# Kernel optimization log

Measured on AMD Instinct MI355X. Metric: run time of the kernel, lower is better.

## Reference

```python
import jax, jax.numpy as jnp
import numpy as np

N, E, D_IN, D_OUT = 100000, 1600000, 128, 128
EPS = 1e-12  # torch F.normalize clamp


def setup_inputs() -> dict:
    key = jax.random.key(0)
    ks = jax.random.split(key, 8)
    return {
        "x": jax.random.normal(ks[0], (N, D_IN), dtype=jnp.float32),
        "edge_src": jax.random.randint(ks[1], (E,), 0, N, dtype=jnp.int32),
        "edge_dst": jax.random.randint(ks[2], (E,), 0, N, dtype=jnp.int32),
        "edge_weight": jax.random.uniform(ks[3], (E,), dtype=jnp.float32),
        "W_l": jax.random.normal(ks[4], (D_IN, D_OUT), dtype=jnp.float32) / np.sqrt(D_IN),
        "b_l": jax.random.normal(ks[5], (D_OUT,), dtype=jnp.float32) * 0.01,
        "W_r": jax.random.normal(ks[6], (D_IN, D_OUT), dtype=jnp.float32) / np.sqrt(D_IN),
        "b_r": jax.random.normal(ks[7], (D_OUT,), dtype=jnp.float32) * 0.01,
    }


def reference(x, edge_src, edge_dst, edge_weight, W_l, b_l, W_r, b_r):
    # spmm(adj, x): weighted gather of source node features, scatter-add to targets
    agg = jax.ops.segment_sum(x[edge_src] * edge_weight[:, None], edge_dst,
                              num_segments=x.shape[0])          # [N, D_IN]
    out = agg @ W_l + b_l + (x @ W_r + b_r)                      # lin_l + lin_r (num_tgt == N)
    # L1 normalize along features (F.normalize, p=1, dim=1)
    l1 = jnp.maximum(jnp.sum(jnp.abs(out), axis=1, keepdims=True), EPS)
    return out / l1
```

## Files before the change

kernel.cpp:

```cpp
#include <hip/hip_runtime.h>
#include <hip/hip_fp16.h>


static constexpr int D = 128;
static constexpr int CBITS = 6;
static constexpr int CSZ = 1 << CBITS;
static constexpr int NB = 2048;
static constexpr int NPART = 256;

typedef _Float16 half8 __attribute__((ext_vector_type(8)));
typedef float f32x4 __attribute__((ext_vector_type(4)));

__global__ __launch_bounds__(256) void prep(
    const int* __restrict__ edst, int* __restrict__ bhist, int E, int chunk,
    const float4* __restrict__ x4, __half2* __restrict__ xh2, int n4,
    const float* __restrict__ Wl, const float* __restrict__ Wr,
    __half* __restrict__ wt, int do_cvt)
{
    __shared__ int hist[NB];
    const int b = blockIdx.x;
    const int tid = threadIdx.x;
    if (b < NPART) {
        for (int t = tid; t < NB; t += 256) hist[t] = 0;
        __syncthreads();
        const int beg = b * chunk;
        const int end = min(E, beg + chunk);
        int e = beg + tid;
        for (; e + 3 * 256 < end; e += 4 * 256) {
            const int d0 = edst[e];
            const int d1 = edst[e + 256];
            const int d2 = edst[e + 512];
            const int d3 = edst[e + 768];
            atomicAdd(&hist[d0 >> CBITS], 1);
            atomicAdd(&hist[d1 >> CBITS], 1);
            atomicAdd(&hist[d2 >> CBITS], 1);
            atomicAdd(&hist[d3 >> CBITS], 1);
        }
        for (; e < end; e += 256)
            atomicAdd(&hist[edst[e] >> CBITS], 1);
        __syncthreads();
        for (int t = tid; t < NB; t += 256)
            bhist[(size_t)b * NB + t] = hist[t];
    } else if (do_cvt) {
        const int cb = b - NPART;
        if (cb < 1024) {
            int i = cb * 256 + tid;
            const int stride = 1024 * 256;
            for (; i < n4; i += stride) {
                float4 v = x4[i];
                xh2[2 * i + 0] = __floats2half2_rn(v.x, v.y);
                xh2[2 * i + 1] = __floats2half2_rn(v.z, v.w);
            }
        } else {
            const int idx = (cb - 1024) * 256 + tid;
            if (idx < 128 * 256) {
                const int c = idx >> 8;
                const int k = idx & 255;
                const float v = (k < 128) ? Wl[(size_t)k * D + c]
                                          : Wr[(size_t)(k - 128) * D + c];
                wt[(size_t)c * 256 + k] = __float2half(v);
            }
        }
    }
}

__global__ __launch_bounds__(64) void bucket_scan(
    int* __restrict__ bhist, int* __restrict__ ctot)
{
    const int t = blockIdx.x * 64 + threadIdx.x;
    int run = 0;
    for (int b = 0; b < NPART; b += 8) {
        int v[8];
#pragma unroll
        for (int i = 0; i < 8; ++i)
            v[i] = bhist[(size_t)(b + i) * NB + t];
#pragma unroll
        for (int i = 0; i < 8; ++i) {
            const int c = v[i];
            bhist[(size_t)(b + i) * NB + t] = run;
            run += c;
        }
    }
    ctot[t] = run;
}

__global__ __launch_bounds__(1024) void coarse_scan(
    const int* __restrict__ ctot, int* __restrict__ cbase,
    int* __restrict__ offs, int N, int E)
{
    __shared__ int s[1024];
    const int t = threadIdx.x;
    const int v0 = ctot[2 * t];
    const int v1 = ctot[2 * t + 1];
    const int loc = v0 + v1;
    s[t] = loc;
    __syncthreads();
    for (int off = 1; off < 1024; off <<= 1) {
        const int u = (t >= off) ? s[t - off] : 0;
        __syncthreads();
        s[t] += u;
        __syncthreads();
    }
    const int excl = s[t] - loc;
    cbase[2 * t]     = excl;
    cbase[2 * t + 1] = excl + v0;
    if (t == 1023) { cbase[NB] = s[t]; offs[N] = E; }
}

__global__ __launch_bounds__(256) void coarse_partition(
    const int* __restrict__ esrc, const int* __restrict__ edst,
    const float* __restrict__ ew, const int* __restrict__ bhist,
    const int* __restrict__ cbase,
    int2* __restrict__ cpairs, int E, int chunk)
{
    __shared__ int cur[NB];
    for (int t = threadIdx.x; t < NB; t += 256)
        cur[t] = bhist[(size_t)blockIdx.x * NB + t] + cbase[t];
    __syncthreads();
    const int beg = blockIdx.x * chunk;
    const int end = min(E, beg + chunk);
    int e = beg + threadIdx.x;
    for (; e + 3 * 256 < end; e += 4 * 256) {
        int d_[4], s_[4]; float w_[4];
#pragma unroll
        for (int i = 0; i < 4; ++i) {
            d_[i] = edst[e + i * 256];
            s_[i] = esrc[e + i * 256];
            w_[i] = ew[e + i * 256];
        }
#pragma unroll
        for (int i = 0; i < 4; ++i) {
            const int pos = atomicAdd(&cur[d_[i] >> CBITS], 1);
            cpairs[pos] = make_int2(((d_[i] & (CSZ - 1)) << 20) | s_[i],
                                    __float_as_int(w_[i]));
        }
    }
    for (; e < end; e += 256) {
        const int d = edst[e];
        const int pos = atomicAdd(&cur[d >> CBITS], 1);
        cpairs[pos] = make_int2(((d & (CSZ - 1)) << 20) | esrc[e],
                                __float_as_int(ew[e]));
    }
}

__global__ __launch_bounds__(256) void fine_sort(
    const int2* __restrict__ cpairs, const int* __restrict__ cbase,
    int* __restrict__ offs, int2* __restrict__ pairs, int N)
{
    __shared__ int hist[CSZ], scn[CSZ], cur[CSZ];
    const int b = blockIdx.x;
    const int t = threadIdx.x;
    const int lane = t & 63;
    const int s0 = cbase[b], s1 = cbase[b + 1];
    if (t < CSZ) hist[t] = 0;
    __syncthreads();
    for (int i = s0 + t; i < s1; i += 256)
        atomicAdd(&hist[(cpairs[i].x >> 20) & (CSZ - 1)], 1);
    __syncthreads();
    if (t < CSZ) {
        const int v = hist[t];
        int xs = v;
#pragma unroll
        for (int off = 1; off < 64; off <<= 1) {
            const int y = __shfl_up(xs, off, 64);
            if (lane >= off) xs += y;
        }
        const int base = s0 + xs - v;
        scn[t] = base;
        cur[t] = base;
        const int node = (b << CBITS) + t;
        if (node < N) offs[node] = base;
    }
    __syncthreads();
    for (int i = s0 + t; i < s1; i += 256) {
        const int2 p = cpairs[i];
        const int pos = atomicAdd(&cur[(p.x >> 20) & (CSZ - 1)], 1);
        pairs[pos] = make_int2(p.x & 0xFFFFF, p.y);
    }
}

template <bool FP16X>
__global__ __launch_bounds__(256) void sage_gather(
    const void* __restrict__ xrows,
    const int2* __restrict__ pairs,
    const int* __restrict__ offs,
    void* __restrict__ agg,
    int N)
{
    int node = (blockIdx.x * blockDim.x + threadIdx.x) >> 6;
    const int lane = threadIdx.x & 63;
    if (node >= N) return;
    node = __builtin_amdgcn_readfirstlane(node);
    const int beg = offs[node];
    const int end = offs[node + 1];
    const int sub = lane >> 5;
    const int cl  = lane & 31;

    const __half* __restrict__ xh = (const __half*)xrows;
    const float*  __restrict__ xf = (const float*)xrows;

    float a0 = 0.f, a1 = 0.f, a2 = 0.f, a3 = 0.f;
    int k = beg;
    for (; k + 8 <= end; k += 8) {
        int s_[4]; float w_[4];
#pragma unroll
        for (int i = 0; i < 4; ++i) {
            const int2 ea = pairs[k + 2 * i + 0];
            const int2 eb = pairs[k + 2 * i + 1];
            s_[i] = sub ? eb.x : ea.x;
            w_[i] = __int_as_float(sub ? eb.y : ea.y);
        }
        if (FP16X) {
            float2 raw[4];
#pragma unroll
            for (int i = 0; i < 4; ++i)
                raw[i] = *reinterpret_cast<const float2*>(&xh[(size_t)s_[i] * D + cl * 4]);
#pragma unroll
            for (int i = 0; i < 4; ++i) {
                union { float2 f2; __half2 h[2]; } u;
                u.f2 = raw[i];
                const float2 f01 = __half22float2(u.h[0]);
                const float2 f23 = __half22float2(u.h[1]);
                a0 = fmaf(f01.x, w_[i], a0);
                a1 = fmaf(f01.y, w_[i], a1);
                a2 = fmaf(f23.x, w_[i], a2);
                a3 = fmaf(f23.y, w_[i], a3);
            }
        } else {
            float4 raw[4];
#pragma unroll
            for (int i = 0; i < 4; ++i)
                raw[i] = *reinterpret_cast<const float4*>(&xf[(size_t)s_[i] * D + cl * 4]);
#pragma unroll
            for (int i = 0; i < 4; ++i) {
                a0 = fmaf(raw[i].x, w_[i], a0);
                a1 = fmaf(raw[i].y, w_[i], a1);
                a2 = fmaf(raw[i].z, w_[i], a2);
                a3 = fmaf(raw[i].w, w_[i], a3);
            }
        }
    }
    for (int t = 0; k + t < end; ++t) {
        if (sub == (t & 1)) {
            const int2 p = pairs[k + t];
            const float w = __int_as_float(p.y);
            if (FP16X) {
                union { float2 f2; __half2 h[2]; } u;
                u.f2 = *reinterpret_cast<const float2*>(&xh[(size_t)p.x * D + cl * 4]);
                const float2 f01 = __half22float2(u.h[0]);
                const float2 f23 = __half22float2(u.h[1]);
                a0 = fmaf(f01.x, w, a0); a1 = fmaf(f01.y, w, a1);
                a2 = fmaf(f23.x, w, a2); a3 = fmaf(f23.y, w, a3);
            } else {
                const float4 v = *reinterpret_cast<const float4*>(&xf[(size_t)p.x * D + cl * 4]);
                a0 = fmaf(v.x, w, a0); a1 = fmaf(v.y, w, a1);
                a2 = fmaf(v.z, w, a2); a3 = fmaf(v.w, w, a3);
            }
        }
    }
    a0 += __shfl_xor(a0, 32, 64);
    a1 += __shfl_xor(a1, 32, 64);
    a2 += __shfl_xor(a2, 32, 64);
    a3 += __shfl_xor(a3, 32, 64);

    if (sub == 0) {
        if (FP16X) {
            union { __half2 h[2]; int2 i2; } u;
            u.h[0] = __floats2half2_rn(a0, a1);
            u.h[1] = __floats2half2_rn(a2, a3);
            *reinterpret_cast<int2*>(&((__half*)agg)[(size_t)node * D + cl * 4]) = u.i2;
        } else {
            *reinterpret_cast<float4*>(&((float*)agg)[(size_t)node * D + cl * 4]) =
                make_float4(a0, a1, a2, a3);
        }
    }
}

__global__ __launch_bounds__(256) void sage_scatter(
    const float* __restrict__ x,
    const int* __restrict__ esrc,
    const int* __restrict__ edst,
    const float* __restrict__ ew,
    float* agg, int E)
{
    const int lane = threadIdx.x & 63;
    const int warp = (blockIdx.x * blockDim.x + threadIdx.x) >> 6;
    const int nwarps = (gridDim.x * blockDim.x) >> 6;
    const float2* __restrict__ x2 = reinterpret_cast<const float2*>(x);
    for (int e = warp; e < E; e += nwarps) {
        const int s = esrc[e];
        const int d = edst[e];
        const float w = ew[e];
        const float2 xv = x2[s * 64 + lane];
        atomicAdd(&agg[d * D + lane * 2 + 0], xv.x * w);
        atomicAdd(&agg[d * D + lane * 2 + 1], xv.y * w);
    }
}

__global__ __launch_bounds__(256) void sage_linear_norm_mfma(
    const __half* __restrict__ aggh,
    const __half* __restrict__ xh,
    const __half* __restrict__ wt,
    const float* __restrict__ bl,
    const float* __restrict__ br,
    float* __restrict__ out,
    int N)
{
    __shared__ __half a_s[64][136];
    __shared__ __half w_s[128][136];
    const int tid = threadIdx.x;
    const int bn = blockIdx.x * 64;
    const int wv = tid >> 6;
    const int l  = tid & 63;
    const int lr = l & 15;
    const int lq = l >> 4;

    f32x4 acc[8];
#pragma unroll
    for (int t = 0; t < 8; ++t) acc[t] = f32x4{0.f, 0.f, 0.f, 0.f};

    const int ar  = tid >> 2;
    const int as  = (tid & 3) * 32;
    const int wr  = tid >> 1;
    const int wsg = (tid & 1) * 64;

#pragma unroll
    for (int c = 0; c < 2; ++c) {
        const __half* __restrict__ A = c ? xh : aggh;
        __syncthreads();
        {
            const int gn = bn + ar;
            half8 v0 = {}, v1 = {}, v2 = {}, v3 = {};
            if (gn < N) {
                const half8* src = reinterpret_cast<const half8*>(&A[(size_t)gn * D + as]);
                v0 = src[0]; v1 = src[1]; v2 = src[2]; v3 = src[3];
            }
            half8* dst = reinterpret_cast<half8*>(&a_s[ar][as]);
            dst[0] = v0; dst[1] = v1; dst[2] = v2; dst[3] = v3;
        }
        {
            const half8* src = reinterpret_cast<const half8*>(&wt[(size_t)wr * 256 + c * 128 + wsg]);
            half8* dst = reinterpret_cast<half8*>(&w_s[wr][wsg]);
#pragma unroll
            for (int j = 0; j < 8; ++j) dst[j] = src[j];
        }
        __syncthreads();

#pragma unroll
        for (int ks = 0; ks < 4; ++ks) {
            const int k0 = ks * 32 + lq * 8;
            const half8 af = *reinterpret_cast<const half8*>(&a_s[wv * 16 + lr][k0]);
#pragma unroll
            for (int t = 0; t < 8; ++t) {
                const half8 bf = *reinterpret_cast<const half8*>(&w_s[t * 16 + lr][k0]);
                acc[t] = __builtin_amdgcn_mfma_f32_16x16x32_f16(af, bf, acc[t], 0, 0, 0);
            }
        }
    }

    float bias[8];
#pragma unroll
    for (int t = 0; t < 8; ++t) {
        const int cidx = t * 16 + lr;
        bias[t] = bl[cidx] + br[cidx];
    }
    float v[8][4];
    float s0 = 0.f, s1 = 0.f, s2 = 0.f, s3 = 0.f;
#pragma unroll
    for (int t = 0; t < 8; ++t) {
        v[t][0] = acc[t][0] + bias[t];
        v[t][1] = acc[t][1] + bias[t];
        v[t][2] = acc[t][2] + bias[t];
        v[t][3] = acc[t][3] + bias[t];
        s0 += fabsf(v[t][0]); s1 += fabsf(v[t][1]);
        s2 += fabsf(v[t][2]); s3 += fabsf(v[t][3]);
    }
#pragma unroll
    for (int m = 1; m < 16; m <<= 1) {
        s0 += __shfl_xor(s0, m, 64);
        s1 += __shfl_xor(s1, m, 64);
        s2 += __shfl_xor(s2, m, 64);
        s3 += __shfl_xor(s3, m, 64);
    }
    const float r0 = 1.0f / fmaxf(s0, 1e-12f);
    const float r1 = 1.0f / fmaxf(s1, 1e-12f);
    const float r2 = 1.0f / fmaxf(s2, 1e-12f);
    const float r3 = 1.0f / fmaxf(s3, 1e-12f);

    const int nd0 = bn + wv * 16 + lq * 4;
#pragma unroll
    for (int r = 0; r < 4; ++r) {
        const int nd = nd0 + r;
        if (nd < N) {
            const float ri = (r == 0) ? r0 : (r == 1) ? r1 : (r == 2) ? r2 : r3;
#pragma unroll
            for (int t = 0; t < 8; ++t)
                out[(size_t)nd * D + t * 16 + lr] = v[t][r] * ri;
        }
    }
}

__global__ __launch_bounds__(256) void sage_linear_norm(
    const float* agg, const float* __restrict__ x,
    const float* __restrict__ Wl, const float* __restrict__ bl,
    const float* __restrict__ Wr, const float* __restrict__ br,
    float* out, int N)
{
    __shared__ float a_s[64][68];
    __shared__ float w_s[64][132];
    const int tid = threadIdx.x;
    const int jg = tid & 31;
    const int ng = tid >> 5;
    const int bn = blockIdx.x * 64;

    float acc[8][4];
#pragma unroll
    for (int i = 0; i < 8; ++i) {
        acc[i][0] = 0.f; acc[i][1] = 0.f; acc[i][2] = 0.f; acc[i][3] = 0.f;
    }
    const int sn  = tid >> 2;
    const int skb = (tid & 3) << 4;
    const int wr  = tid >> 5;
    const int wc  = (tid & 31) << 2;

    for (int c = 0; c < 4; ++c) {
        const float* A = (c < 2) ? agg : x;
        const float* __restrict__ W = (c < 2) ? Wl : Wr;
        const int kb = (c & 1) << 6;
        __syncthreads();
        const int gn = bn + sn;
#pragma unroll
        for (int it = 0; it < 4; ++it) {
            float4 vv = make_float4(0.f, 0.f, 0.f, 0.f);
            if (gn < N)
                vv = *reinterpret_cast<const float4*>(&A[(size_t)gn * D + kb + skb + it * 4]);
            *reinterpret_cast<float4*>(&a_s[sn][skb + it * 4]) = vv;
        }
#pragma unroll
        for (int it = 0; it < 8; ++it) {
            const int row = it * 8 + wr;
            const float4 vv = *reinterpret_cast<const float4*>(&W[(size_t)(kb + row) * D + wc]);
            *reinterpret_cast<float4*>(&w_s[row][wc]) = vv;
        }
        __syncthreads();
#pragma unroll 4
        for (int kk = 0; kk < 64; kk += 4) {
            const float4 w0 = *reinterpret_cast<const float4*>(&w_s[kk + 0][jg << 2]);
            const float4 w1 = *reinterpret_cast<const float4*>(&w_s[kk + 1][jg << 2]);
            const float4 w2 = *reinterpret_cast<const float4*>(&w_s[kk + 2][jg << 2]);
            const float4 w3 = *reinterpret_cast<const float4*>(&w_s[kk + 3][jg << 2]);
#pragma unroll
            for (int i = 0; i < 8; ++i) {
                const float4 av = *reinterpret_cast<const float4*>(&a_s[(ng << 3) + i][kk]);
                acc[i][0] = fmaf(av.w, w3.x, fmaf(av.z, w2.x, fmaf(av.y, w1.x, fmaf(av.x, w0.x, acc[i][0]))));
                acc[i][1] = fmaf(av.w, w3.y, fmaf(av.z, w2.y, fmaf(av.y, w1.y, fmaf(av.x, w0.y, acc[i][1]))));
                acc[i][2] = fmaf(av.w, w3.z, fmaf(av.z, w2.z, fmaf(av.y, w1.z, fmaf(av.x, w0.z, acc[i][2]))));
                acc[i][3] = fmaf(av.w, w3.w, fmaf(av.z, w2.w, fmaf(av.y, w1.w, fmaf(av.x, w0.w, acc[i][3]))));
            }
        }
    }
    const float4 bl4 = *reinterpret_cast<const float4*>(&bl[jg << 2]);
    const float4 br4 = *reinterpret_cast<const float4*>(&br[jg << 2]);
    const float bx = bl4.x + br4.x, by = bl4.y + br4.y,
                bz = bl4.z + br4.z, bw = bl4.w + br4.w;
#pragma unroll
    for (int i = 0; i < 8; ++i) {
        const float v0 = acc[i][0] + bx;
        const float v1 = acc[i][1] + by;
        const float v2 = acc[i][2] + bz;
        const float v3 = acc[i][3] + bw;
        float s = fabsf(v0) + fabsf(v1) + fabsf(v2) + fabsf(v3);
#pragma unroll
        for (int m = 1; m < 32; m <<= 1) s += __shfl_xor(s, m, 64);
        s = fmaxf(s, 1e-12f);
        const float r = 1.0f / s;
        const int n = bn + (ng << 3) + i;
        if (n < N) {
            const float4 o = make_float4(v0 * r, v1 * r, v2 * r, v3 * r);
            *reinterpret_cast<float4*>(&out[(size_t)n * D + (jg << 2)]) = o;
        }
    }
}

extern "C" void kernel_launch(void* const* d_in, const int* in_sizes, int n_in,
                              void* d_out, int out_size, void* d_ws, size_t ws_size,
                              hipStream_t stream) {
    const float* x    = (const float*)d_in[0];
    const int*   esrc = (const int*)  d_in[1];
    const int*   edst = (const int*)  d_in[2];
    const float* ew   = (const float*)d_in[3];
    const float* Wl   = (const float*)d_in[4];
    const float* bl   = (const float*)d_in[5];
    const float* Wr   = (const float*)d_in[6];
    const float* br   = (const float*)d_in[7];
    float* out = (float*)d_out;

    const int N = in_sizes[0] / D;
    const int E = in_sizes[1];

    auto align256 = [](size_t v) { return (v + 255) & ~size_t(255); };
    size_t off_bhist  = 0;
    size_t off_ctot   = align256(off_bhist  + (size_t)NPART * NB * 4);
    size_t off_cbase  = align256(off_ctot   + (size_t)NB * 4);
    size_t off_offs   = align256(off_cbase  + (size_t)(NB + 1) * 4);
    size_t off_cpairs = align256(off_offs   + (size_t)(N + 1) * 4);
    size_t off_pairs  = align256(off_cpairs + (size_t)E * 8);
    size_t off_xh     = align256(off_pairs  + (size_t)E * 8);
    size_t off_aggh   = align256(off_xh     + (size_t)N * D * 2);
    size_t off_wt     = align256(off_aggh   + (size_t)N * D * 2);
    size_t need_b     = off_xh;
    size_t need_a     = off_wt + (size_t)256 * D * 2;

    const int nbu = (N + CSZ - 1) >> CBITS;
    const bool fits_meta = (N <= (1 << 20)) && (nbu <= NB);

    if (ws_size >= need_b && fits_meta) {
        char* ws = (char*)d_ws;
        int*  bhist  = (int*) (ws + off_bhist);
        int*  ctot   = (int*) (ws + off_ctot);
        int*  cbase  = (int*) (ws + off_cbase);
        int*  offs   = (int*) (ws + off_offs);
        int2* cpairs = (int2*)(ws + off_cpairs);
        int2* pairs  = (int2*)(ws + off_pairs);
        __half2* xh  = (__half2*)(ws + off_xh);
        __half*  agh = (__half*)(ws + off_aggh);
        __half*  wt  = (__half*)(ws + off_wt);

        const bool mfma = (ws_size >= need_a);
        const int chunk = (E + NPART - 1) / NPART;

        const int prep_grid = NPART + (mfma ? (1024 + 128) : 0);
        prep<<<prep_grid, 256, 0, stream>>>(edst, bhist, E, chunk,
                                            (const float4*)x, xh, N * (D / 4),
                                            Wl, Wr, wt, mfma ? 1 : 0);
        bucket_scan<<<NB / 64, 64, 0, stream>>>(bhist, ctot);
        coarse_scan<<<1, 1024, 0, stream>>>(ctot, cbase, offs, N, E);
        coarse_partition<<<NPART, 256, 0, stream>>>(esrc, edst, ew, bhist, cbase,
                                                    cpairs, E, chunk);
        fine_sort<<<nbu, 256, 0, stream>>>(cpairs, cbase, offs, pairs, N);

        const int gb = (N * 64 + 255) / 256;
        const int nb = (N + 63) / 64;
        if (mfma) {
            sage_gather<true ><<<gb, 256, 0, stream>>>(xh, pairs, offs, agh, N);
            sage_linear_norm_mfma<<<nb, 256, 0, stream>>>(agh, (const __half*)xh, wt,
                                                          bl, br, out, N);
        } else {
            sage_gather<false><<<gb, 256, 0, stream>>>(x, pairs, offs, out, N);
            sage_linear_norm<<<nb, 256, 0, stream>>>(out, x, Wl, bl, Wr, br, out, N);
        }
    } else {
        hipMemsetAsync(out, 0, (size_t)N * D * sizeof(float), stream);
        sage_scatter<<<2048, 256, 0, stream>>>(x, esrc, edst, ew, out, E);
        const int nb = (N + 63) / 64;
        sage_linear_norm<<<nb, 256, 0, stream>>>(out, x, Wl, bl, Wr, br, out, N);
    }
}
```

Measured before the change: 149.3 us.

## Use full-wave row gather per edge and wave-shuffle scan in coarse_scan

The gather kernel now has all 64 lanes cooperate on one source row per edge, each lane loading a half2 or float2, instead of splitting the wave into two half-waves that each handle alternate edges with 4-wide loads. This drops the cross-half shuffle reduction and the per-lane edge selection, at the cost of narrower per-lane loads and one row in flight per edge step. The coarse scan replaces a shared-memory Hillis-Steele scan that needed many barriers with wave-level shuffle scans plus one small scan over wave sums. The scan kernel is tiny, so most of the effect depends on how the gather's memory access pattern changes.

Result: faster. 146.0 us, median of 2 (-2.2%).

```diff
diff --git a/kernel.cpp b/kernel.cpp
--- a/kernel.cpp
+++ b/kernel.cpp
@@ -88,23 +88,36 @@
     const int* __restrict__ ctot, int* __restrict__ cbase,
     int* __restrict__ offs, int N, int E)
 {
-    __shared__ int s[1024];
+    __shared__ int wsum[16];
     const int t = threadIdx.x;
+    const int lane = t & 63;
+    const int wv = t >> 6;
     const int v0 = ctot[2 * t];
     const int v1 = ctot[2 * t + 1];
     const int loc = v0 + v1;
-    s[t] = loc;
+    int xs = loc;
+#pragma unroll
+    for (int off = 1; off < 64; off <<= 1) {
+        const int y = __shfl_up(xs, off, 64);
+        if (lane >= off) xs += y;
+    }
+    if (lane == 63) wsum[wv] = xs;
     __syncthreads();
-    for (int off = 1; off < 1024; off <<= 1) {
-        const int u = (t >= off) ? s[t - off] : 0;
-        __syncthreads();
-        s[t] += u;
-        __syncthreads();
-    }
-    const int excl = s[t] - loc;
+    if (t < 16) {
+        const int w = wsum[t];
+        int ws = w;
+#pragma unroll
+        for (int off = 1; off < 16; off <<= 1) {
+            const int y = __shfl_up(ws, off, 64);
+            if (lane >= off) ws += y;
+        }
+        wsum[t] = ws - w;
+    }
+    __syncthreads();
+    const int excl = wsum[wv] + xs - loc;
     cbase[2 * t]     = excl;
     cbase[2 * t + 1] = excl + v0;
-    if (t == 1023) { cbase[NB] = s[t]; offs[N] = E; }
+    if (t == 1023) { cbase[NB] = excl + loc; offs[N] = E; }
 }
 
 __global__ __launch_bounds__(256) void coarse_partition(
@@ -193,86 +206,50 @@
     node = __builtin_amdgcn_readfirstlane(node);
     const int beg = offs[node];
     const int end = offs[node + 1];
-    const int sub = lane >> 5;
-    const int cl  = lane & 31;
-
-    const __half* __restrict__ xh = (const __half*)xrows;
-    const float*  __restrict__ xf = (const float*)xrows;
-
-    float a0 = 0.f, a1 = 0.f, a2 = 0.f, a3 = 0.f;
+
+    const __half2* __restrict__ xh = (const __half2*)xrows;
+    const float2*  __restrict__ xf = (const float2*)xrows;
+
+    float ax0 = 0.f, ay0 = 0.f, ax1 = 0.f, ay1 = 0.f;
     int k = beg;
-    for (; k + 8 <= end; k += 8) {
-        int s_[4]; float w_[4];
-#pragma unroll
-        for (int i = 0; i < 4; ++i) {
-            const int2 ea = pairs[k + 2 * i + 0];
-            const int2 eb = pairs[k + 2 * i + 1];
-            s_[i] = sub ? eb.x : ea.x;
-            w_[i] = __int_as_float(sub ? eb.y : ea.y);
-        }
+    for (; k + 4 <= end; k += 4) {
+        const int2 p0 = pairs[k + 0];
+        const int2 p1 = pairs[k + 1];
+        const int2 p2 = pairs[k + 2];
+        const int2 p3 = pairs[k + 3];
+        float2 v0, v1, v2, v3;
         if (FP16X) {
-            float2 raw[4];
-#pragma unroll
-            for (int i = 0; i < 4; ++i)
-                raw[i] = *reinterpret_cast<const float2*>(&xh[(size_t)s_[i] * D + cl * 4]);
-#pragma unroll
-            for (int i = 0; i < 4; ++i) {
-                union { float2 f2; __half2 h[2]; } u;
-                u.f2 = raw[i];
-                const float2 f01 = __half22float2(u.h[0]);
-                const float2 f23 = __half22float2(u.h[1]);
-                a0 = fmaf(f01.x, w_[i], a0);
-                a1 = fmaf(f01.y, w_[i], a1);
-                a2 = fmaf(f23.x, w_[i], a2);
-                a3 = fmaf(f23.y, w_[i], a3);
-            }
+            v0 = __half22float2(xh[(size_t)p0.x * 64 + lane]);
+            v1 = __half22float2(xh[(size_t)p1.x * 64 + lane]);
+            v2 = __half22float2(xh[(size_t)p2.x * 64 + lane]);
+            v3 = __half22float2(xh[(size_t)p3.x * 64 + lane]);
         } else {
-            float4 raw[4];
-#pragma unroll
-            for (int i = 0; i < 4; ++i)
-                raw[i] = *reinterpret_cast<const float4*>(&xf[(size_t)s_[i] * D + cl * 4]);
-#pragma unroll
-            for (int i = 0; i < 4; ++i) {
-                a0 = fmaf(raw[i].x, w_[i], a0);
-                a1 = fmaf(raw[i].y, w_[i], a1);
-                a2 = fmaf(raw[i].z, w_[i], a2);
-                a3 = fmaf(raw[i].w, w_[i], a3);
-            }
-        }
-    }
-    for (int t = 0; k + t < end; ++t) {
-        if (sub == (t & 1)) {
-            const int2 p = pairs[k + t];
-            const float w = __int_as_float(p.y);
-            if (FP16X) {
-                union { float2 f2; __half2 h[2]; } u;
-                u.f2 = *reinterpret_cast<const float2*>(&xh[(size_t)p.x * D + cl * 4]);
-                const float2 f01 = __half22float2(u.h[0]);
-                const float2 f23 = __half22float2(u.h[1]);
-                a0 = fmaf(f01.x, w, a0); a1 = fmaf(f01.y, w, a1);
-                a2 = fmaf(f23.x, w, a2); a3 = fmaf(f23.y, w, a3);
-            } else {
-                const float4 v = *reinterpret_cast<const float4*>(&xf[(size_t)p.x * D + cl * 4]);
-                a0 = fmaf(v.x, w, a0); a1 = fmaf(v.y, w, a1);
-                a2 = fmaf(v.z, w, a2); a3 = fmaf(v.w, w, a3);
-            }
-        }
-    }
-    a0 += __shfl_xor(a0, 32, 64);
-    a1 += __shfl_xor(a1, 32, 64);
-    a2 += __shfl_xor(a2, 32, 64);
-    a3 += __shfl_xor(a3, 32, 64);
-
-    if (sub == 0) {
-        if (FP16X) {
-            union { __half2 h[2]; int2 i2; } u;
-            u.h[0] = __floats2half2_rn(a0, a1);
-            u.h[1] = __floats2half2_rn(a2, a3);
-            *reinterpret_cast<int2*>(&((__half*)agg)[(size_t)node * D + cl * 4]) = u.i2;
-        } else {
-            *reinterpret_cast<float4*>(&((float*)agg)[(size_t)node * D + cl * 4]) =
-                make_float4(a0, a1, a2, a3);
-        }
+            v0 = xf[(size_t)p0.x * 64 + lane];
+            v1 = xf[(size_t)p1.x * 64 + lane];
+            v2 = xf[(size_t)p2.x * 64 + lane];
+            v3 = xf[(size_t)p3.x * 64 + lane];
+        }
+        const float w0 = __int_as_float(p0.y), w1 = __int_as_float(p1.y);
+        const float w2 = __int_as_float(p2.y), w3 = __int_as_float(p3.y);
+        ax0 = fmaf(v0.x, w0, ax0); ay0 = fmaf(v0.y, w0, ay0);
+        ax1 = fmaf(v1.x, w1, ax1); ay1 = fmaf(v1.y, w1, ay1);
+        ax0 = fmaf(v2.x, w2, ax0); ay0 = fmaf(v2.y, w2, ay0);
+        ax1 = fmaf(v3.x, w3, ax1); ay1 = fmaf(v3.y, w3, ay1);
+    }
+    for (; k < end; ++k) {
+        const int2 p = pairs[k];
+        const float w = __int_as_float(p.y);
+        float2 v;
+        if (FP16X) v = __half22float2(xh[(size_t)p.x * 64 + lane]);
+        else       v = xf[(size_t)p.x * 64 + lane];
+        ax0 = fmaf(v.x, w, ax0); ay0 = fmaf(v.y, w, ay0);
+    }
+    const float ax = ax0 + ax1;
+    const float ay = ay0 + ay1;
+    if (FP16X) {
+        ((__half2*)agg)[(size_t)node * 64 + lane] = __floats2half2_rn(ax, ay);
+    } else {
+        ((float2*)agg)[(size_t)node * 64 + lane] = make_float2(ax, ay);
     }
 }
 
```
